# Performance work log

Hardware: AMD Instinct MI355X
Metric: run time of the kernel (lower is better)

## Reference

```python
import jax, jax.numpy as jnp
import numpy as np

MODES = 16

def setup_inputs() -> dict:
    key = jax.random.key(0)
    k1, k2 = jax.random.split(key)
    x = jax.random.normal(k1, (16, 32, 256, 256), dtype=jnp.float32)
    weights = jax.random.normal(k2, (32, 32, MODES, MODES, 2), dtype=jnp.float32) * 0.1
    return {"x": x, "weights": weights}

def reference(x, weights):
    # x: [B, Ci, H, W]; weights: [Ci, Co, m, m, 2]
    B, Ci, H, W = x.shape
    m = weights.shape[2]
    Co = weights.shape[1]
    x_ft = jnp.fft.rfft2(x, axes=(-2, -1))  # [B, Ci, H, W//2+1] complex
    w_c = jax.lax.complex(weights[..., 0], weights[..., 1])  # [Ci, Co, m, m]
    low = jnp.einsum('bixy,ioxy->boxy', x_ft[:, :, :m, :m], w_c)  # [B, Co, m, m]
    out_ft = jnp.zeros((B, Co, H, W // 2 + 1), dtype=x_ft.dtype)
    out_ft = out_ft.at[:, :, :m, :m].set(low)
    return jnp.fft.irfft2(out_ft, s=(H, W), axes=(-2, -1)).astype(x.dtype)
```

## Files before the change

### kernel.cpp

```cpp
#include <hip/hip_runtime.h>

typedef float v4 __attribute__((ext_vector_type(4)));
typedef float f32x4 __attribute__((ext_vector_type(4)));
typedef short bf16x8 __attribute__((ext_vector_type(8)));

#define TWO_PI_256 0.024543692606170259f


__device__ __forceinline__ unsigned short f2bf(float f) {
  const unsigned int u = __float_as_uint(f);
  return (unsigned short)((u + 0x7fffu + ((u >> 16) & 1u)) >> 16);
}
__device__ __forceinline__ float bf2f(unsigned short h) {
  return __uint_as_float(((unsigned int)h) << 16);
}

__global__ __launch_bounds__(256) void k0_trig(unsigned short* __restrict__ Th,
                                               unsigned short* __restrict__ Tl) {
  const int k = threadIdx.x;
#pragma unroll
  for (int kx = 0; kx < 16; ++kx) {
    float sv, cv;
    sincosf((float)((kx * k) & 255) * TWO_PI_256, &sv, &cv);
    const float vals[2] = {cv, -sv};
#pragma unroll
    for (int p = 0; p < 2; ++p) {
      const int o = 2 * kx + p;
      const unsigned short hi = f2bf(vals[p]);
      Th[o * 256 + k] = hi;
      Tl[o * 256 + k] = f2bf(vals[p] - bf2f(hi));
    }
  }
}

typedef __attribute__((address_space(1))) const unsigned int gas_u32;
typedef __attribute__((address_space(3))) unsigned int las_u32;

__global__ __launch_bounds__(256) void k1_dftw(const float* __restrict__ x,
                                               const unsigned short* __restrict__ Th,
                                               const unsigned short* __restrict__ Tl,
                                               float* __restrict__ F) {
  __shared__ float Xs[128 * 32];
  __shared__ __align__(16) unsigned short Ts[2][32 * 264];
  const int tid = threadIdx.x;
  const int lane = tid & 63;
  const int w = tid >> 6;
  const long rblk = (long)blockIdx.x * 128;
  {
    const int o = tid >> 3, kb = (tid & 7) * 32;
#pragma unroll
    for (int f = 0; f < 2; ++f) {
      const unsigned short* src = (f ? Tl : Th) + o * 256 + kb;
      unsigned short* dst = &Ts[f][o * 264 + kb];
#pragma unroll
      for (int j = 0; j < 32; j += 8)
        *(bf16x8*)(dst + j) = *(const bf16x8*)(src + j);
    }
  }
  const int q = lane >> 4;
  const int n16 = lane & 15;
  f32x4 acc[2][2] = {};
  for (int kc = 0; kc < 256; kc += 32) {
    __syncthreads();
#pragma unroll
    for (int i = 0; i < 4; ++i) {
      const int r0 = w * 32 + i * 8;
      __builtin_amdgcn_global_load_lds(
          (gas_u32*)(x + (rblk + r0 + (lane >> 3)) * 256 + kc + (lane & 7) * 4),
          (las_u32*)((unsigned int*)Xs + r0 * 32), 16, 0, 0);
    }
    __syncthreads();
    bf16x8 bh[2], bl[2];
#pragma unroll
    for (int nt = 0; nt < 2; ++nt) {
      const int o = nt * 16 + n16;
      bh[nt] = *(const bf16x8*)&Ts[0][o * 264 + kc + q * 8];
      bl[nt] = *(const bf16x8*)&Ts[1][o * 264 + kc + q * 8];
    }
#pragma unroll
    for (int mt = 0; mt < 2; ++mt) {
      const int m = w * 32 + mt * 16 + n16;
      const float* ap = &Xs[m * 32 + q * 8];
      const v4 a0 = *(const v4*)ap;
      const v4 a1 = *(const v4*)(ap + 4);
      const float af[8] = {a0[0], a0[1], a0[2], a0[3], a1[0], a1[1], a1[2], a1[3]};
      bf16x8 ah, al;
#pragma unroll
      for (int j = 0; j < 8; ++j) {
        const unsigned short h = f2bf(af[j]);
        ah[j] = (short)h;
        al[j] = (short)f2bf(af[j] - bf2f(h));
      }
#pragma unroll
      for (int nt = 0; nt < 2; ++nt) {
        acc[mt][nt] = __builtin_amdgcn_mfma_f32_16x16x32_bf16(ah, bh[nt], acc[mt][nt], 0, 0, 0);
        acc[mt][nt] = __builtin_amdgcn_mfma_f32_16x16x32_bf16(al, bh[nt], acc[mt][nt], 0, 0, 0);
        acc[mt][nt] = __builtin_amdgcn_mfma_f32_16x16x32_bf16(ah, bl[nt], acc[mt][nt], 0, 0, 0);
      }
    }
  }
#pragma unroll
  for (int mt = 0; mt < 2; ++mt)
#pragma unroll
    for (int nt = 0; nt < 2; ++nt)
#pragma unroll
      for (int r = 0; r < 4; ++r) {
        const long row = rblk + w * 32 + mt * 16 + q * 4 + r;
        F[row * 32 + nt * 16 + n16] = acc[mt][nt][r];
      }
}

__global__ __launch_bounds__(256) void k2_dfth(const float* __restrict__ F,
                                               float* __restrict__ X) {
  __shared__ float2 tbl[256];
  __shared__ float Fs[64][36];
  const int tid = threadIdx.x;
  const int bc = blockIdx.x;
  {
    float sv, cv;
    sincosf((float)tid * TWO_PI_256, &sv, &cv);
    tbl[tid] = make_float2(cv, sv);
  }
  const int kx = tid & 15;
  const int ky = tid >> 4;
  float xr = 0.f, xi = 0.f;
  const float* Fb = F + (long)bc * 8192;
  for (int hc = 0; hc < 256; hc += 64) {
    __syncthreads();
#pragma unroll
    for (int p = 0; p < 2; ++p) {
      const int h = (tid >> 3) + p * 32;
      const int j = (tid & 7) * 4;
      *(v4*)&Fs[h][j] = *(const v4*)&Fb[(hc + h) * 32 + j];
    }
    __syncthreads();
#pragma unroll 8
    for (int hl = 0; hl < 64; ++hl) {
      const int h = hc + hl;
      const float2 f = *(const float2*)&Fs[hl][2 * kx];
      const float2 w = tbl[(ky * h) & 255];
      xr += f.x * w.x + f.y * w.y;
      xi += f.y * w.x - f.x * w.y;
    }
  }
  *(float2*)&X[((long)bc * 256 + tid) * 2] = make_float2(xr, xi);
}

__global__ __launch_bounds__(256) void k3_mix(const float* __restrict__ X,
                                              const float* __restrict__ Wt,
                                              float* __restrict__ Y) {
  const int t = threadIdx.x;
  const int co = blockIdx.x;
  const int b = blockIdx.y;
  float yr = 0.f, yi = 0.f;
#pragma unroll 4
  for (int ci = 0; ci < 32; ++ci) {
    const float2 xv = *(const float2*)&X[((long)(b * 32 + ci) * 256 + t) * 2];
    const float2 wv = *(const float2*)&Wt[((long)(ci * 32 + co) * 256 + t) * 2];
    yr += xv.x * wv.x - xv.y * wv.y;
    yi += xv.x * wv.y + xv.y * wv.x;
  }
  *(float2*)&Y[((long)(b * 32 + co) * 256 + t) * 2] = make_float2(yr, yi);
}

__global__ __launch_bounds__(256) void k4_inv(const float* __restrict__ Y,
                                              float* __restrict__ out) {
  __shared__ float2 tbl[256];
  __shared__ float2 Ys[256];
  __shared__ float G[256][36];
  const int tid = threadIdx.x;
  const int co = blockIdx.x;
  const int b = blockIdx.y;
  {
    float sv, cv;
    sincosf((float)tid * TWO_PI_256, &sv, &cv);
    tbl[tid] = make_float2(cv, sv);
  }
  Ys[tid] = *(const float2*)&Y[((long)(b * 32 + co) * 256 + tid) * 2];
  __syncthreads();
  {
    float gr[16] = {}, gi[16] = {};
#pragma unroll 4
    for (int ky = 0; ky < 16; ++ky) {
      const float2 w = tbl[(ky * tid) & 255];
#pragma unroll
      for (int kx = 0; kx < 16; ++kx) {
        const float2 yv = Ys[ky * 16 + kx];
        gr[kx] += yv.x * w.x - yv.y * w.y;
        gi[kx] += yv.x * w.y + yv.y * w.x;
      }
    }
#pragma unroll
    for (int kx = 0; kx < 16; ++kx)
      *(float2*)&G[tid][2 * kx] = make_float2(gr[kx], gi[kx]);
  }
  __syncthreads();
  const int s = tid & 127;
  const int hh = tid >> 7;
  float cs[16], sn[16];
#pragma unroll
  for (int kx = 1; kx < 16; ++kx) {
    const float2 w = tbl[(kx * s) & 255];
    cs[kx] = 2.f * w.x;
    sn[kx] = 2.f * w.y;
  }
  const float inv = 1.f / 65536.f;
  float* __restrict__ ob = out + (long)(b * 32 + co) * 65536;
  for (int h = hh; h < 256; h += 2) {
    float gr[16], gi[16];
#pragma unroll
    for (int j = 0; j < 8; ++j) {
      const v4 qv = *(const v4*)&G[h][4 * j];
      gr[2 * j] = qv[0];
      gi[2 * j] = qv[1];
      gr[2 * j + 1] = qv[2];
      gi[2 * j + 1] = qv[3];
    }
    float a = gr[0];
    float bs = 0.f;
#pragma unroll
    for (int kx = 1; kx < 16; ++kx) {
      a += gr[kx] * cs[kx];
      bs += gi[kx] * sn[kx];
    }
    if (s == 0) {
      float a128 = gr[0];
#pragma unroll
      for (int kx = 1; kx < 16; ++kx)
        a128 += (kx & 1) ? -2.f * gr[kx] : 2.f * gr[kx];
      ob[h * 256] = a * inv;
      ob[h * 256 + 128] = a128 * inv;
    } else {
      ob[h * 256 + s] = (a - bs) * inv;
      ob[h * 256 + 256 - s] = (a + bs) * inv;
    }
  }
}

extern "C" void kernel_launch(void* const* d_in, const int* in_sizes, int n_in,
                              void* d_out, int out_size, void* d_ws, size_t ws_size,
                              hipStream_t stream) {
  const float* x = (const float*)d_in[0];
  const float* wt = (const float*)d_in[1];
  float* out = (float*)d_out;
  float* F = (float*)d_ws;
  float* X = F + 4194304;
  float* Yv = X + 262144;
  unsigned short* Th = (unsigned short*)(Yv + 262144);
  unsigned short* Tl = Th + 8192;
  k0_trig<<<1, 256, 0, stream>>>(Th, Tl);
  k1_dftw<<<1024, 256, 0, stream>>>(x, Th, Tl, F);
  k2_dfth<<<512, 256, 0, stream>>>(F, X);
  k3_mix<<<dim3(32, 16), 256, 0, stream>>>(X, wt, Yv);
  k4_inv<<<dim3(32, 16), 256, 0, stream>>>(Yv, out);
}
```

Before: 296.2 us.

## Compute inverse W-direction DFT in k4 with split-bf16 MFMA and double grid

The inverse real DFT along W, previously a scalar FMA loop with symmetric output writes, becomes a matrix multiply of G (rows × 32 real/imag coefficients) against a precomputed basis matrix. That basis, pre-swizzled and scaled, is built in k0 as hi/lo bf16 pairs and fed to 3-term bf16 MFMA for near-fp32 accuracy. Each k4 block now covers half the H rows, doubling the grid to 1024 blocks for more parallelism and less shared memory. This adds basis-table reads from global memory and a large set of accumulators, which raises register pressure.

```diff
diff --git a/kernel.cpp b/kernel.cpp
--- a/kernel.cpp
+++ b/kernel.cpp
@@ -16,7 +16,9 @@
 }
 
 __global__ __launch_bounds__(256) void k0_trig(unsigned short* __restrict__ Th,
-                                               unsigned short* __restrict__ Tl) {
+                                               unsigned short* __restrict__ Tl,
+                                               unsigned short* __restrict__ Bh,
+                                               unsigned short* __restrict__ Bl) {
   const int k = threadIdx.x;
 #pragma unroll
   for (int kx = 0; kx < 16; ++kx) {
@@ -30,6 +32,29 @@
       Th[o * 256 + k] = hi;
       Tl[o * 256 + k] = f2bf(vals[p] - bf2f(hi));
     }
+  }
+  for (int idx = threadIdx.x; idx < 8192; idx += 256) {
+    const int nt = idx >> 9;
+    const int lane = (idx >> 3) & 63;
+    const int j = idx & 7;
+    const int q = lane >> 4;
+    const int n16 = lane & 15;
+    const int kk = q * 8 + j;
+    const int w = nt * 16 + n16;
+    float val;
+    if (kk == 0) {
+      val = 1.f / 65536.f;
+    } else if (kk == 16) {
+      val = 0.f;
+    } else {
+      const int kx = kk & 15;
+      float sv, cv;
+      sincosf((float)((kx * w) & 255) * TWO_PI_256, &sv, &cv);
+      val = (kk < 16 ? 2.f * cv : -2.f * sv) * (1.f / 65536.f);
+    }
+    const unsigned short hi = f2bf(val);
+    Bh[idx] = hi;
+    Bl[idx] = f2bf(val - bf2f(hi));
   }
 }
 
@@ -164,77 +189,87 @@
 }
 
 __global__ __launch_bounds__(256) void k4_inv(const float* __restrict__ Y,
+                                              const unsigned short* __restrict__ Bh,
+                                              const unsigned short* __restrict__ Bl,
                                               float* __restrict__ out) {
   __shared__ float2 tbl[256];
   __shared__ float2 Ys[256];
-  __shared__ float G[256][36];
+  __shared__ float Gs[128][36];
   const int tid = threadIdx.x;
-  const int co = blockIdx.x;
+  const int lane = tid & 63;
+  const int wv = tid >> 6;
+  const int co = blockIdx.x >> 1;
+  const int h0 = (blockIdx.x & 1) << 7;
   const int b = blockIdx.y;
+  const long bc = b * 32 + co;
   {
     float sv, cv;
     sincosf((float)tid * TWO_PI_256, &sv, &cv);
     tbl[tid] = make_float2(cv, sv);
   }
-  Ys[tid] = *(const float2*)&Y[((long)(b * 32 + co) * 256 + tid) * 2];
+  Ys[tid] = *(const float2*)&Y[(bc * 256 + tid) * 2];
   __syncthreads();
   {
-    float gr[16] = {}, gi[16] = {};
+    const int hl = tid >> 1;
+    const int p = tid & 1;
+    const int h = h0 + hl;
+    float gr[8] = {}, gi[8] = {};
 #pragma unroll 4
     for (int ky = 0; ky < 16; ++ky) {
-      const float2 w = tbl[(ky * tid) & 255];
-#pragma unroll
-      for (int kx = 0; kx < 16; ++kx) {
-        const float2 yv = Ys[ky * 16 + kx];
-        gr[kx] += yv.x * w.x - yv.y * w.y;
-        gi[kx] += yv.x * w.y + yv.y * w.x;
-      }
-    }
-#pragma unroll
-    for (int kx = 0; kx < 16; ++kx)
-      *(float2*)&G[tid][2 * kx] = make_float2(gr[kx], gi[kx]);
+      const float2 wt = tbl[(ky * h) & 255];
+#pragma unroll
+      for (int i = 0; i < 8; ++i) {
+        const float2 yv = Ys[ky * 16 + p * 8 + i];
+        gr[i] += yv.x * wt.x - yv.y * wt.y;
+        gi[i] += yv.x * wt.y + yv.y * wt.x;
+      }
+    }
+#pragma unroll
+    for (int i = 0; i < 8; ++i) {
+      const int kx = p * 8 + i;
+      Gs[hl][kx] = gr[i];
+      Gs[hl][16 + kx] = gi[i];
+    }
   }
   __syncthreads();
-  const int s = tid & 127;
-  const int hh = tid >> 7;
-  float cs[16], sn[16];
-#pragma unroll
-  for (int kx = 1; kx < 16; ++kx) {
-    const float2 w = tbl[(kx * s) & 255];
-    cs[kx] = 2.f * w.x;
-    sn[kx] = 2.f * w.y;
-  }
-  const float inv = 1.f / 65536.f;
-  float* __restrict__ ob = out + (long)(b * 32 + co) * 65536;
-  for (int h = hh; h < 256; h += 2) {
-    float gr[16], gi[16];
+  const int q = lane >> 4;
+  const int n16 = lane & 15;
+  bf16x8 ah[2], al[2];
+#pragma unroll
+  for (int mt = 0; mt < 2; ++mt) {
+    const float* ap = &Gs[wv * 32 + mt * 16 + n16][q * 8];
+    const v4 a0 = *(const v4*)ap;
+    const v4 a1 = *(const v4*)(ap + 4);
+    const float af[8] = {a0[0], a0[1], a0[2], a0[3], a1[0], a1[1], a1[2], a1[3]};
 #pragma unroll
     for (int j = 0; j < 8; ++j) {
-      const v4 qv = *(const v4*)&G[h][4 * j];
-      gr[2 * j] = qv[0];
-      gi[2 * j] = qv[1];
-      gr[2 * j + 1] = qv[2];
-      gi[2 * j + 1] = qv[3];
-    }
-    float a = gr[0];
-    float bs = 0.f;
-#pragma unroll
-    for (int kx = 1; kx < 16; ++kx) {
-      a += gr[kx] * cs[kx];
-      bs += gi[kx] * sn[kx];
-    }
-    if (s == 0) {
-      float a128 = gr[0];
-#pragma unroll
-      for (int kx = 1; kx < 16; ++kx)
-        a128 += (kx & 1) ? -2.f * gr[kx] : 2.f * gr[kx];
-      ob[h * 256] = a * inv;
-      ob[h * 256 + 128] = a128 * inv;
-    } else {
-      ob[h * 256 + s] = (a - bs) * inv;
-      ob[h * 256 + 256 - s] = (a + bs) * inv;
-    }
-  }
+      const unsigned short hh = f2bf(af[j]);
+      ah[mt][j] = (short)hh;
+      al[mt][j] = (short)f2bf(af[j] - bf2f(hh));
+    }
+  }
+  f32x4 acc[2][16] = {};
+#pragma unroll
+  for (int nt = 0; nt < 16; ++nt) {
+    const bf16x8 bhf = *(const bf16x8*)&Bh[(nt * 64 + lane) * 8];
+    const bf16x8 blf = *(const bf16x8*)&Bl[(nt * 64 + lane) * 8];
+#pragma unroll
+    for (int mt = 0; mt < 2; ++mt) {
+      acc[mt][nt] = __builtin_amdgcn_mfma_f32_16x16x32_bf16(ah[mt], bhf, acc[mt][nt], 0, 0, 0);
+      acc[mt][nt] = __builtin_amdgcn_mfma_f32_16x16x32_bf16(al[mt], bhf, acc[mt][nt], 0, 0, 0);
+      acc[mt][nt] = __builtin_amdgcn_mfma_f32_16x16x32_bf16(ah[mt], blf, acc[mt][nt], 0, 0, 0);
+    }
+  }
+  float* __restrict__ ob = out + bc * 65536;
+#pragma unroll
+  for (int mt = 0; mt < 2; ++mt)
+#pragma unroll
+    for (int r = 0; r < 4; ++r) {
+      const int h = h0 + wv * 32 + mt * 16 + q * 4 + r;
+#pragma unroll
+      for (int nt = 0; nt < 16; ++nt)
+        ob[h * 256 + nt * 16 + n16] = acc[mt][nt][r];
+    }
 }
 
 extern "C" void kernel_launch(void* const* d_in, const int* in_sizes, int n_in,
@@ -248,9 +283,11 @@
   float* Yv = X + 262144;
   unsigned short* Th = (unsigned short*)(Yv + 262144);
   unsigned short* Tl = Th + 8192;
-  k0_trig<<<1, 256, 0, stream>>>(Th, Tl);
+  unsigned short* Bh = Tl + 8192;
+  unsigned short* Bl = Bh + 8192;
+  k0_trig<<<1, 256, 0, stream>>>(Th, Tl, Bh, Bl);
   k1_dftw<<<1024, 256, 0, stream>>>(x, Th, Tl, F);
   k2_dfth<<<512, 256, 0, stream>>>(F, X);
   k3_mix<<<dim3(32, 16), 256, 0, stream>>>(X, wt, Yv);
-  k4_inv<<<dim3(32, 16), 256, 0, stream>>>(Yv, out);
-}
+  k4_inv<<<dim3(64, 16), 256, 0, stream>>>(Yv, Bh, Bl, out);
+}
```

New measurement: 303.2 us. 2.4% more time.
